# Optimization experiments

Hardware: AMD Instinct MI355X
Metric: run time of the kernel (lower is better)

The kernel has to match this reference:

```python
import jax, jax.numpy as jnp
import numpy as np


def _log_g(x):
    # log of g(x) = x + 0.5 for x >= 0, sigmoid(x) for x < 0 (minGRU paper, log-space)
    return jnp.where(x >= 0, jnp.log(jax.nn.relu(x) + 0.5), -jax.nn.softplus(-x))


def setup_inputs() -> dict:
    key = jax.random.key(0)
    k1, k2, k3 = jax.random.split(key, 3)
    B, L, D, H = 4, 8192, 512, 1024
    x = jax.random.normal(k1, (B, L, D), dtype=jnp.float32)
    # 1x1 conv in-projection to [hidden | gate], scaled for sane activation magnitudes
    W_in = jax.random.normal(k2, (2 * H, D), dtype=jnp.float32) * 0.05
    b_in = jnp.zeros((2 * H,), dtype=jnp.float32)
    # 1x1 conv out-projection back to model dim
    W_out = jax.random.normal(k3, (D, H), dtype=jnp.float32) * 0.05
    b_out = jnp.zeros((D,), dtype=jnp.float32)
    return {"x": x, "W_in": W_in, "b_in": b_in, "W_out": W_out, "b_out": b_out}


def reference(x, W_in, b_in, W_out, b_out):
    # x: [B, L, D]. tokenMixer transposes to [B, D, L] for MinGRU (1x1 convs),
    # which is equivalent to pointwise matmuls over the channel dim here.
    hg = jnp.einsum('bld,ed->ble', x, W_in) + b_in          # [B, L, 2H]
    H = hg.shape[-1] // 2
    hidden, gate = hg[..., :H], hg[..., H:]

    # minGRU log-space parallel scan (Heinsen associative scan):
    # h_t = (1 - z_t) * h_{t-1} + z_t * g(hidden_t), z_t = sigmoid(gate_t)
    log_coeffs = -jax.nn.softplus(gate)      # log(1 - z_t)
    log_z = -jax.nn.softplus(-gate)          # log(z_t)
    log_tilde_h = _log_g(hidden)             # log(g(hidden_t))

    a_star = jnp.cumsum(log_coeffs, axis=1)                              # [B, L, H]
    log_h = a_star + jax.lax.cumlogsumexp(log_z + log_tilde_h - a_star, axis=1)
    h = jnp.exp(log_h)                                                   # [B, L, H]

    out = jnp.einsum('blh,dh->bld', h, W_out) + b_out                    # [B, L, D]
    return out
```

## Files before the change

kernel.cpp:

```cpp
#include <hip/hip_runtime.h>
#include <hip/hip_bf16.h>
#include <cstdint>
#include <cstddef>

#define B_ 4
#define L_ 8192
#define D_ 512
#define H_ 1024
#define NC_ 256
#define LC_ (L_ / NC_)

typedef float  f32x4 __attribute__((ext_vector_type(4)));
typedef short  s16x8 __attribute__((ext_vector_type(8)));
typedef __bf16 b16x8 __attribute__((ext_vector_type(8)));

template <typename T, typename U>
__device__ inline auto mfma_sel(T a, T b, f32x4 c, U, int)
    -> decltype(__builtin_amdgcn_mfma_f32_16x16x32_bf16(a, b, c, 0, 0, 0)) {
  return __builtin_amdgcn_mfma_f32_16x16x32_bf16(a, b, c, 0, 0, 0);
}
template <typename T, typename U>
__device__ inline f32x4 mfma_sel(T a, T b, f32x4 c, U, long) {
  return __builtin_amdgcn_mfma_f32_16x16x32_bf16(
      __builtin_bit_cast(U, a), __builtin_bit_cast(U, b), c, 0, 0, 0);
}
__device__ inline f32x4 mfma_bf16_16x16x32(s16x8 a, s16x8 b, f32x4 c) {
  return mfma_sel(a, b, c, b16x8{}, 0);
}

__device__ inline ushort f2bf(float f) {
  uint32_t u = __builtin_bit_cast(uint32_t, f);
  uint32_t r = (u + 0x7fffu + ((u >> 16) & 1u)) >> 16;
  return (ushort)r;
}
__device__ inline float bf2f(ushort u) {
  return __builtin_bit_cast(float, (uint32_t)u << 16);
}

__device__ inline float softplus_f(float x) {
  return fmaxf(x, 0.f) + __logf(1.f + __expf(-fabsf(x)));
}
__device__ inline float logaddexp_f(float a, float b) {
  float m = fmaxf(a, b);
  return m + __logf(1.f + __expf(-fabsf(a - b)));
}
__device__ inline void transform_f(float hd, float g, float& lc, float& v) {
  float sp = softplus_f(g);
  lc = -sp;
  float lz = g - sp;
  float lth = (hd >= 0.f) ? __logf(hd + 0.5f) : (hd - softplus_f(hd));
  v = lz + lth;
}

__global__ void cast_kernel(const float* __restrict__ in, ushort* __restrict__ out, int n4) {
  int i = blockIdx.x * blockDim.x + threadIdx.x;
  if (i >= n4) return;
  float4 f = reinterpret_cast<const float4*>(in)[i];
  ushort4 o;
  o.x = f2bf(f.x); o.y = f2bf(f.y); o.z = f2bf(f.z); o.w = f2bf(f.w);
  reinterpret_cast<ushort4*>(out)[i] = o;
}

__global__ void cast2_kernel(const float* __restrict__ in0, ushort* __restrict__ out0, int n4_0,
                             const float* __restrict__ in1, ushort* __restrict__ out1, int n4_1) {
  int i = blockIdx.x * blockDim.x + threadIdx.x;
  const float* in; ushort* out;
  if (i < n4_0) { in = in0; out = out0; }
  else { i -= n4_0; if (i >= n4_1) return; in = in1; out = out1; }
  float4 f = reinterpret_cast<const float4*>(in)[i];
  ushort4 o;
  o.x = f2bf(f.x); o.y = f2bf(f.y); o.z = f2bf(f.z); o.w = f2bf(f.w);
  reinterpret_cast<ushort4*>(out)[i] = o;
}

#define GLDS(srcp, dstp)                                                            \
  __builtin_amdgcn_global_load_lds(                                                 \
      (const __attribute__((address_space(1))) void*)(srcp),                        \
      (__attribute__((address_space(3))) void*)(dstp), 16, 0, 0)

template <int MODE>
__global__ __launch_bounds__(256, 3)
void gemm_bt(const ushort* __restrict__ A, const ushort* __restrict__ Bm,
             const float* __restrict__ bias, void* __restrict__ Cv,
             int M, int N, int K) {
  __shared__ ushort As[128 * 64];
  __shared__ ushort Bs[128 * 64];
  const int tid  = threadIdx.x;
  const int wave = tid >> 6;
  const int lane = tid & 63;
  const int l15  = lane & 15;
  const int quad = lane >> 4;

  int id = blockIdx.y * gridDim.x + blockIdx.x;
  const int nwg = gridDim.x * gridDim.y;
  id = (id & 7) * (nwg >> 3) + (id >> 3);
  const int bxi = id % gridDim.x;
  const int byi = id / gridDim.x;

  const long bm = (long)byi * 128;
  const int  wm = (wave >> 1) * 64;

  f32x4 acc[4][4];
#pragma unroll
  for (int i = 0; i < 4; ++i)
#pragma unroll
    for (int j = 0; j < 4; ++j) acc[i][j] = (f32x4){0.f, 0.f, 0.f, 0.f};

  const int rl  = lane >> 3;
  const int cb  = (lane & 7) ^ rl;
  const ushort* gA0 = A + (bm + wave * 32 + rl) * (long)K + cb * 8;
  long bRowBase;
  if (MODE == 1) {
    const long n0 = (long)bxi * 64;
    bRowBase = (wave < 2) ? (n0 + wave * 32) : (1024 + n0 + (wave - 2) * 32);
  } else {
    bRowBase = (long)bxi * 128 + wave * 32;
  }
  const ushort* gB0 = Bm + (bRowBase + rl) * (long)K + cb * 8;
  ushort* lA[4]; ushort* lB[4];
#pragma unroll
  for (int i = 0; i < 4; ++i) {
    lA[i] = &As[(wave * 32 + 8 * i) * 64];
    lB[i] = &Bs[(wave * 32 + 8 * i) * 64];
  }

  const int sq0 = ((0 * 4 + quad) ^ (l15 & 7)) * 8;
  const int sq1 = ((1 * 4 + quad) ^ (l15 & 7)) * 8;
  int arow[4], brow[4];
#pragma unroll
  for (int i = 0; i < 4; ++i) arow[i] = (wm + i * 16 + l15) * 64;
  if (MODE == 1) {
    const int wn0 = (wave & 1) * 32;
#pragma unroll
    for (int j = 0; j < 4; ++j) {
      const int trow = (j < 2) ? (wn0 + j * 16) : (64 + wn0 + (j - 2) * 16);
      brow[j] = (trow + l15) * 64;
    }
  } else {
    const int wn = (wave & 1) * 64;
#pragma unroll
    for (int j = 0; j < 4; ++j) brow[j] = (wn + j * 16 + l15) * 64;
  }

  for (int k0 = 0; k0 < K; k0 += 64) {
#pragma unroll
    for (int i = 0; i < 4; ++i)
      GLDS(gA0 + 8L * i * K + k0, lA[i]);
#pragma unroll
    for (int i = 0; i < 4; ++i)
      GLDS(gB0 + 8L * i * K + k0, lB[i]);
    __syncthreads();

#pragma unroll
    for (int kh = 0; kh < 2; ++kh) {
      const int sq = kh ? sq1 : sq0;
      s16x8 af[4], bf[4];
#pragma unroll
      for (int mi = 0; mi < 4; ++mi)
        af[mi] = *reinterpret_cast<const s16x8*>(&As[arow[mi] + sq]);
#pragma unroll
      for (int ni = 0; ni < 4; ++ni)
        bf[ni] = *reinterpret_cast<const s16x8*>(&Bs[brow[ni] + sq]);
      __builtin_amdgcn_s_setprio(1);
#pragma unroll
      for (int mi = 0; mi < 4; ++mi)
#pragma unroll
        for (int ni = 0; ni < 4; ++ni)
          acc[mi][ni] = mfma_bf16_16x16x32(af[mi], bf[ni], acc[mi][ni]);
      __builtin_amdgcn_s_setprio(0);
    }
    __syncthreads();
  }

  if (MODE == 1) {
    const long n0  = (long)bxi * 64;
    const int  wn0 = (wave & 1) * 32;
#pragma unroll
    for (int mi = 0; mi < 4; ++mi) {
      const long mrow = bm + wm + mi * 16 + quad * 4;
#pragma unroll
      for (int j = 0; j < 2; ++j) {
        const long ch = n0 + wn0 + j * 16 + l15;
        const float bh = bias[ch];
        const float bg = bias[1024 + ch];
        ushort* lp = (ushort*)Cv + mrow * (long)N + ch;
#pragma unroll
        for (int r = 0; r < 4; ++r) {
          float hd = acc[mi][j][r] + bh;
          float g  = acc[mi][j + 2][r] + bg;
          float lc, v; transform_f(hd, g, lc, v);
          lp[(long)r * N] = f2bf(lc);
          lp[(long)r * N + 1024] = f2bf(v);
        }
      }
    }
  } else {
    const int wn = (wave & 1) * 64;
#pragma unroll
    for (int mi = 0; mi < 4; ++mi) {
      const long mrow = bm + wm + mi * 16 + quad * 4;
#pragma unroll
      for (int ni = 0; ni < 4; ++ni) {
        const long ncol = (long)bxi * 128 + wn + ni * 16 + l15;
        const float bv = bias[ncol];
        float* cp = (float*)Cv + mrow * (long)N + ncol;
#pragma unroll
        for (int r = 0; r < 4; ++r) cp[(long)r * N] = acc[mi][ni][r] + bv;
      }
    }
  }
}

__global__ void scan_phase1(const ushort* __restrict__ hg,
                            float* __restrict__ Ac, float* __restrict__ Bc) {
  int gid = blockIdx.x * blockDim.x + threadIdx.x;
  int hq = gid & (H_ / 4 - 1);
  int c  = (gid >> 8) & (NC_ - 1);
  int b  = gid >> 16;
  const ushort* p = hg + ((size_t)(b * L_ + c * LC_) * (2 * H_)) + hq * 4;
  float As[4] = {0.f, 0.f, 0.f, 0.f};
  float Bv[4] = {-INFINITY, -INFINITY, -INFINITY, -INFINITY};
#pragma unroll 4
  for (int l = 0; l < LC_; ++l) {
    ushort4 lc4 = *reinterpret_cast<const ushort4*>(p);
    ushort4 v4  = *reinterpret_cast<const ushort4*>(p + H_);
    float lcv[4] = {bf2f(lc4.x), bf2f(lc4.y), bf2f(lc4.z), bf2f(lc4.w)};
    float vv[4]  = {bf2f(v4.x),  bf2f(v4.y),  bf2f(v4.z),  bf2f(v4.w)};
#pragma unroll
    for (int j = 0; j < 4; ++j) {
      As[j] += lcv[j];
      Bv[j] = logaddexp_f(Bv[j] + lcv[j], vv[j]);
    }
    p += 2 * H_;
  }
  size_t o = (size_t)(b * NC_ + c) * H_ + hq * 4;
  *reinterpret_cast<float4*>(&Ac[o]) = make_float4(As[0], As[1], As[2], As[3]);
  *reinterpret_cast<float4*>(&Bc[o]) = make_float4(Bv[0], Bv[1], Bv[2], Bv[3]);
}

__global__ void scan_phase2(const float* __restrict__ Ac, const float* __restrict__ Bc,
                            float* __restrict__ carry) {
  int gid = blockIdx.x * blockDim.x + threadIdx.x;
  int h = gid & (H_ - 1);
  int b = gid >> 10;
  float P = -INFINITY;
  for (int c = 0; c < NC_; ++c) {
    size_t o = (size_t)(b * NC_ + c) * H_ + h;
    carry[o] = P;
    P = logaddexp_f(P + Ac[o], Bc[o]);
  }
}

__global__ void scan_phase3(const ushort* __restrict__ hg, const float* __restrict__ carry,
                            ushort* __restrict__ hb) {
  int gid = blockIdx.x * blockDim.x + threadIdx.x;
  int hq = gid & (H_ / 4 - 1);
  int c  = (gid >> 8) & (NC_ - 1);
  int b  = gid >> 16;
  float4 cr = *reinterpret_cast<const float4*>(&carry[(size_t)(b * NC_ + c) * H_ + hq * 4]);
  float lh[4] = {cr.x, cr.y, cr.z, cr.w};
  const ushort* p = hg + ((size_t)(b * L_ + c * LC_) * (2 * H_)) + hq * 4;
  ushort* q = hb + (size_t)(b * L_ + c * LC_) * H_ + hq * 4;
#pragma unroll 4
  for (int l = 0; l < LC_; ++l) {
    ushort4 lc4 = *reinterpret_cast<const ushort4*>(p);
    ushort4 v4  = *reinterpret_cast<const ushort4*>(p + H_);
    float lcv[4] = {bf2f(lc4.x), bf2f(lc4.y), bf2f(lc4.z), bf2f(lc4.w)};
    float vv[4]  = {bf2f(v4.x),  bf2f(v4.y),  bf2f(v4.z),  bf2f(v4.w)};
    ushort4 o;
    ushort* op = &o.x;
#pragma unroll
    for (int j = 0; j < 4; ++j) {
      lh[j] = logaddexp_f(lh[j] + lcv[j], vv[j]);
      op[j] = f2bf(__expf(lh[j]));
    }
    *reinterpret_cast<ushort4*>(q) = o;
    p += 2 * H_;
    q += H_;
  }
}

extern "C" void kernel_launch(void* const* d_in, const int* in_sizes, int n_in,
                              void* d_out, int out_size, void* d_ws, size_t ws_size,
                              hipStream_t stream) {
  const float* x     = (const float*)d_in[0];
  const float* W_in  = (const float*)d_in[1];
  const float* b_in  = (const float*)d_in[2];
  const float* W_out = (const float*)d_in[3];
  const float* b_out = (const float*)d_in[4];
  float* out = (float*)d_out;

  char* ws = (char*)d_ws;
  size_t off = 0;
  auto alloc = [&](size_t bytes) {
    void* p = ws + off;
    off = (off + bytes + 255) & ~(size_t)255;
    return p;
  };
  ushort* xb    = (ushort*)alloc((size_t)B_ * L_ * H_ * 2);
  ushort* hb    = xb;
  ushort* Wib   = (ushort*)alloc((size_t)2 * H_ * D_ * 2);
  ushort* Wob   = (ushort*)alloc((size_t)D_ * H_ * 2);
  ushort* hgb   = (ushort*)alloc((size_t)B_ * L_ * 2 * H_ * 2);
  float*  Ac    = (float*)alloc((size_t)B_ * NC_ * H_ * 4);
  float*  Bc    = (float*)alloc((size_t)B_ * NC_ * H_ * 4);
  float*  carry = (float*)alloc((size_t)B_ * NC_ * H_ * 4);

  cast_kernel<<<(B_ * L_ * D_ / 4 + 255) / 256, 256, 0, stream>>>(x, xb, B_ * L_ * D_ / 4);
  {
    int n0 = 2 * H_ * D_ / 4, n1 = D_ * H_ / 4;
    cast2_kernel<<<(n0 + n1 + 255) / 256, 256, 0, stream>>>(W_in, Wib, n0, W_out, Wob, n1);
  }

  gemm_bt<1><<<dim3(16, (B_ * L_) / 128), 256, 0, stream>>>(
      xb, Wib, b_in, hgb, B_ * L_, 2 * H_, D_);

  scan_phase1<<<(B_ * NC_ * H_ / 4) / 256, 256, 0, stream>>>(hgb, Ac, Bc);
  scan_phase2<<<(B_ * H_) / 256, 256, 0, stream>>>(Ac, Bc, carry);
  scan_phase3<<<(B_ * NC_ * H_ / 4) / 256, 256, 0, stream>>>(hgb, carry, hb);

  gemm_bt<0><<<dim3(D_ / 128, (B_ * L_) / 128), 256, 0, stream>>>(
      hb, Wob, b_out, out, B_ * L_, D_, H_);
}
```

Measured before the change: 367.9 us.

## Fuse chunk scan reduction into input GEMM epilogue and parallelize carry scan

Computes the per-chunk (32-row) sum of log coefficients and logaddexp summary inside the in-projection GEMM epilogue using lane shuffles, removing the separate scan_phase1 pass that re-read the full hg tensor. The sequential carry scan is rewritten as one wave per (batch, channel) doing a warp-level shuffle prefix scan over the 256 chunks. The cost is extra epilogue ALU work and register pressure in the GEMM. Summaries are now built from unrounded fp32 values rather than the bf16 values that phase3 reads back, so chunk carries and intra-chunk recomputation can differ slightly.

```diff
diff --git a/kernel.cpp b/kernel.cpp
--- a/kernel.cpp
+++ b/kernel.cpp
@@ -82,6 +82,7 @@
 __global__ __launch_bounds__(256, 3)
 void gemm_bt(const ushort* __restrict__ A, const ushort* __restrict__ Bm,
              const float* __restrict__ bias, void* __restrict__ Cv,
+             float* __restrict__ Acp, float* __restrict__ Bcp,
              int M, int N, int K) {
   __shared__ ushort As[128 * 64];
   __shared__ ushort Bs[128 * 64];
@@ -175,6 +176,7 @@
   if (MODE == 1) {
     const long n0  = (long)bxi * 64;
     const int  wn0 = (wave & 1) * 32;
+    float sa[4][2], sb[4][2];
 #pragma unroll
     for (int mi = 0; mi < 4; ++mi) {
       const long mrow = bm + wm + mi * 16 + quad * 4;
@@ -184,6 +186,7 @@
         const float bh = bias[ch];
         const float bg = bias[1024 + ch];
         ushort* lp = (ushort*)Cv + mrow * (long)N + ch;
+        float a = 0.f, bb = -INFINITY;
 #pragma unroll
         for (int r = 0; r < 4; ++r) {
           float hd = acc[mi][j][r] + bh;
@@ -191,6 +194,32 @@
           float lc, v; transform_f(hd, g, lc, v);
           lp[(long)r * N] = f2bf(lc);
           lp[(long)r * N + 1024] = f2bf(v);
+          a += lc;
+          bb = logaddexp_f(bb + lc, v);
+        }
+        sa[mi][j] = a; sb[mi][j] = bb;
+      }
+    }
+#pragma unroll
+    for (int j = 0; j < 2; ++j) {
+#pragma unroll
+      for (int cc = 0; cc < 2; ++cc) {
+        float A = 0.f, Bb = -INFINITY;
+#pragma unroll
+        for (int mi = 2 * cc; mi < 2 * cc + 2; ++mi) {
+#pragma unroll
+          for (int q = 0; q < 4; ++q) {
+            float qa = __shfl(sa[mi][j], l15 + 16 * q);
+            float qb = __shfl(sb[mi][j], l15 + 16 * q);
+            Bb = logaddexp_f(Bb + qa, qb);
+            A += qa;
+          }
+        }
+        if (quad == 0) {
+          const long gc = (bm + wm + cc * 32) >> 5;
+          const long ch = n0 + wn0 + j * 16 + l15;
+          Acp[gc * H_ + ch] = A;
+          Bcp[gc * H_ + ch] = Bb;
         }
       }
     }
@@ -211,43 +240,39 @@
   }
 }
 
-__global__ void scan_phase1(const ushort* __restrict__ hg,
-                            float* __restrict__ Ac, float* __restrict__ Bc) {
-  int gid = blockIdx.x * blockDim.x + threadIdx.x;
-  int hq = gid & (H_ / 4 - 1);
-  int c  = (gid >> 8) & (NC_ - 1);
-  int b  = gid >> 16;
-  const ushort* p = hg + ((size_t)(b * L_ + c * LC_) * (2 * H_)) + hq * 4;
-  float As[4] = {0.f, 0.f, 0.f, 0.f};
-  float Bv[4] = {-INFINITY, -INFINITY, -INFINITY, -INFINITY};
-#pragma unroll 4
-  for (int l = 0; l < LC_; ++l) {
-    ushort4 lc4 = *reinterpret_cast<const ushort4*>(p);
-    ushort4 v4  = *reinterpret_cast<const ushort4*>(p + H_);
-    float lcv[4] = {bf2f(lc4.x), bf2f(lc4.y), bf2f(lc4.z), bf2f(lc4.w)};
-    float vv[4]  = {bf2f(v4.x),  bf2f(v4.y),  bf2f(v4.z),  bf2f(v4.w)};
-#pragma unroll
-    for (int j = 0; j < 4; ++j) {
-      As[j] += lcv[j];
-      Bv[j] = logaddexp_f(Bv[j] + lcv[j], vv[j]);
-    }
-    p += 2 * H_;
-  }
-  size_t o = (size_t)(b * NC_ + c) * H_ + hq * 4;
-  *reinterpret_cast<float4*>(&Ac[o]) = make_float4(As[0], As[1], As[2], As[3]);
-  *reinterpret_cast<float4*>(&Bc[o]) = make_float4(Bv[0], Bv[1], Bv[2], Bv[3]);
-}
-
 __global__ void scan_phase2(const float* __restrict__ Ac, const float* __restrict__ Bc,
                             float* __restrict__ carry) {
-  int gid = blockIdx.x * blockDim.x + threadIdx.x;
-  int h = gid & (H_ - 1);
-  int b = gid >> 10;
-  float P = -INFINITY;
-  for (int c = 0; c < NC_; ++c) {
-    size_t o = (size_t)(b * NC_ + c) * H_ + h;
-    carry[o] = P;
-    P = logaddexp_f(P + Ac[o], Bc[o]);
+  const int wid  = (blockIdx.x * blockDim.x + threadIdx.x) >> 6;
+  const int lane = threadIdx.x & 63;
+  const int h = wid & (H_ - 1);
+  const int b = wid >> 10;
+  const size_t base = (size_t)b * NC_ * H_ + h;
+  float pa[4], pb[4];
+#pragma unroll
+  for (int k = 0; k < 4; ++k) {
+    size_t o = base + (size_t)(4 * lane + k) * H_;
+    pa[k] = Ac[o]; pb[k] = Bc[o];
+  }
+  float sA = pa[0], sB = pb[0];
+#pragma unroll
+  for (int k = 1; k < 4; ++k) { sB = logaddexp_f(sB + pa[k], pb[k]); sA += pa[k]; }
+  float iA = sA, iB = sB;
+#pragma unroll
+  for (int d = 1; d < 64; d <<= 1) {
+    float uA = __shfl_up(iA, d);
+    float uB = __shfl_up(iB, d);
+    if (lane >= d) { iB = logaddexp_f(uB + iA, iB); iA = uA + iA; }
+  }
+  float eA = __shfl_up(iA, 1);
+  float eB = __shfl_up(iB, 1);
+  if (lane == 0) { eA = 0.f; eB = -INFINITY; }
+  float Bst = eB, Ast = eA;
+#pragma unroll
+  for (int k = 0; k < 4; ++k) {
+    size_t o = base + (size_t)(4 * lane + k) * H_;
+    carry[o] = Bst;
+    Bst = logaddexp_f(Bst + pa[k], pb[k]);
+    Ast += pa[k];
   }
 }
 
@@ -313,12 +338,11 @@
   }
 
   gemm_bt<1><<<dim3(16, (B_ * L_) / 128), 256, 0, stream>>>(
-      xb, Wib, b_in, hgb, B_ * L_, 2 * H_, D_);
-
-  scan_phase1<<<(B_ * NC_ * H_ / 4) / 256, 256, 0, stream>>>(hgb, Ac, Bc);
-  scan_phase2<<<(B_ * H_) / 256, 256, 0, stream>>>(Ac, Bc, carry);
+      xb, Wib, b_in, hgb, Ac, Bc, B_ * L_, 2 * H_, D_);
+
+  scan_phase2<<<(B_ * H_ * 64) / 256, 256, 0, stream>>>(Ac, Bc, carry);
   scan_phase3<<<(B_ * NC_ * H_ / 4) / 256, 256, 0, stream>>>(hgb, carry, hb);
 
   gemm_bt<0><<<dim3(D_ / 128, (B_ * L_) / 128), 256, 0, stream>>>(
-      hb, Wob, b_out, out, B_ * L_, D_, H_);
-}
+      hb, Wob, b_out, out, nullptr, nullptr, B_ * L_, D_, H_);
+}
```

Result: no change. 365.6 us (-0.6%).
